# Kernel tuning notes

Measured on AMD Instinct MI355X. Metric: run time of the kernel, lower is better.

## Reference

```python
import jax, jax.numpy as jnp
import numpy as np

B, S, D = 2, 2048, 2048
H, G = 32, 8            # n_head, n_kv_groups
DH = D // H             # 64
HG = H // G             # heads per group = 4


def setup_inputs() -> dict:
    key = jax.random.key(0)
    ks = jax.random.split(key, 7)
    kv_dim = G * DH
    return {
        "q": jax.random.normal(ks[0], (B, S, D), jnp.float32),
        "k": jax.random.normal(ks[1], (B, S, D), jnp.float32),
        "v": jax.random.normal(ks[2], (B, S, D), jnp.float32),
        "mask": jnp.tril(jnp.ones((S, S), jnp.bool_)),  # causal
        "w_q": jax.random.normal(ks[3], (D, D), jnp.float32) * 0.02,
        "w_k": jax.random.normal(ks[4], (kv_dim, D), jnp.float32) * 0.02,
        "w_v": jax.random.normal(ks[5], (kv_dim, D), jnp.float32) * 0.02,
        "w_out": jax.random.normal(ks[6], (D, D), jnp.float32) * 0.02,
    }


def reference(q, k, v, mask, w_q, w_k, w_v, w_out):
    scale = 1.0 / np.sqrt(DH).astype(np.float32)
    # projections (F.linear: x @ W.T)
    qp = (q @ w_q.T).reshape(B, S, G, HG, DH)   # [b s g h d]
    kp = (k @ w_k.T).reshape(B, S, G, DH)       # [b t g d]
    vp = (v @ w_v.T).reshape(B, S, G, DH)
    # grouped attention scores [b g h s t]
    scores = jnp.einsum('bsghd,btgd->bghst', qp, kp) * scale
    scores = jnp.where(mask[None, None, None], scores, jnp.float32(-jnp.inf))
    attn = jax.nn.softmax(scores, axis=-1)
    out = jnp.einsum('bghst,btgd->bsghd', attn, vp).reshape(B, S, D)
    return out @ w_out.T
```

## Files before the change

### kernel.cpp

```cpp
#include <hip/hip_runtime.h>
#include <hip/hip_bf16.h>
#include <stdint.h>

#define B_SZ 2
#define S_LEN 2048
#define D_MODEL 2048
#define NH 32
#define NG 8
#define HGRP 4
#define DHEAD 64
#define KV_DIM 512
#define M_TOK 4096
#define KVB 64
#define QBLK 256

typedef __attribute__((ext_vector_type(8))) short bf16x8;
typedef __attribute__((ext_vector_type(4))) float f32x4;
typedef __attribute__((ext_vector_type(16))) float f32x16;

__device__ inline unsigned short f2bf(float x) {
    uint32_t u = __builtin_bit_cast(uint32_t, x);
    uint32_t r = (u + 0x7fffu + ((u >> 16) & 1u)) >> 16;
    return (unsigned short)r;
}

__device__ inline uint32_t cvtpk(float lo, float hi) {
    uint32_t r;
    asm("v_cvt_pk_bf16_f32 %0, %1, %2" : "=v"(r) : "v"(lo), "v"(hi));
    return r;
}

__device__ inline void plswap(uint32_t& a, uint32_t& b) {
    asm volatile("v_permlane32_swap_b32 %0, %1" : "+v"(a), "+v"(b));
}

__device__ inline float bf2f(unsigned short u) {
    uint32_t x = ((uint32_t)u) << 16;
    return __builtin_bit_cast(float, x);
}

__device__ inline void async_copy16(const void* g, void* l) {
    __builtin_amdgcn_global_load_lds(
        (const __attribute__((address_space(1))) void*)g,
        (__attribute__((address_space(3))) void*)l,
        16, 0, 0);
}

__device__ inline void gbar() {
    asm volatile("" ::: "memory");
    __builtin_amdgcn_s_barrier();
    asm volatile("" ::: "memory");
}
__device__ inline void lgkm0() {
    asm volatile("s_waitcnt lgkmcnt(0)" ::: "memory");
    __builtin_amdgcn_sched_barrier(0);
}

__global__ __launch_bounds__(256) void cvt_all(const float* __restrict__ q,
                                               const float* __restrict__ k,
                                               const float* __restrict__ v,
                                               const float* __restrict__ wq,
                                               const float* __restrict__ wk,
                                               const float* __restrict__ wv,
                                               const float* __restrict__ wo,
                                               unsigned short* __restrict__ qb,
                                               unsigned short* __restrict__ kb,
                                               unsigned short* __restrict__ vb,
                                               unsigned short* __restrict__ wqb,
                                               unsigned short* __restrict__ wkvb,
                                               unsigned short* __restrict__ wob) {
    const int i = blockIdx.x * 256 + threadIdx.x;
    const float* src; unsigned short* dst; int j;
    if (i < 1048576)      { src = q;  dst = qb;  j = i; }
    else if (i < 2097152) { src = k;  dst = kb;  j = i - 1048576; }
    else if (i < 3145728) { src = v;  dst = vb;  j = i - 2097152; }
    else if (i < 3670016) { src = wq; dst = wqb; j = i - 3145728; }
    else if (i < 3801088) { src = wk; dst = wkvb; j = i - 3670016; }
    else if (i < 3932160) { src = wv; dst = wkvb + (size_t)KV_DIM * D_MODEL; j = i - 3801088; }
    else                  { src = wo; dst = wob; j = i - 3932160; }
    const float4* p = reinterpret_cast<const float4*>(src) + (size_t)j * 2;
    float4 a = p[0], b = p[1];
    union { unsigned short u[8]; uint4 v4; } r;
    r.u[0] = f2bf(a.x); r.u[1] = f2bf(a.y); r.u[2] = f2bf(a.z); r.u[3] = f2bf(a.w);
    r.u[4] = f2bf(b.x); r.u[5] = f2bf(b.y); r.u[6] = f2bf(b.z); r.u[7] = f2bf(b.w);
    reinterpret_cast<uint4*>(dst)[j] = r.v4;
}

#define SCALE_Q 0.1803368867f
#define GK 2048

__global__ __launch_bounds__(512, 2) void gemm8p(const unsigned short* __restrict__ Aq,
                                                 const unsigned short* __restrict__ Ak,
                                                 const unsigned short* __restrict__ Av,
                                                 const unsigned short* __restrict__ Bq,
                                                 const unsigned short* __restrict__ Bkv,
                                                 unsigned short* __restrict__ out_q,
                                                 unsigned short* __restrict__ out_k,
                                                 unsigned short* __restrict__ out_v) {
    __shared__ __align__(16) char lds[131072];

    const int tid = threadIdx.x;
    const int lane = tid & 63;
    const int w = tid >> 6;
    const int wm = w >> 2, wn = w & 3;
    const int l15 = lane & 15, l4 = lane >> 4;

    int bid = blockIdx.x;
    bid = (bid & 7) * 24 + (bid >> 3);
    const int mb = bid & 15, nb = bid >> 4;
    const int m0 = mb * 256;

    const unsigned short* Ap;
    const unsigned short* Bp;
    int mode = 0, n0q = 0;
    if (nb < 8) {
        Ap = Aq; Bp = Bq + (size_t)(nb * 256) * GK; mode = 0; n0q = nb * 256;
    } else if (nb < 10) {
        Ap = Ak; Bp = Bkv + (size_t)((nb - 8) * 256) * GK; mode = 1; n0q = (nb - 8) * 256;
    } else {
        Ap = Av; Bp = Bkv + (size_t)((nb - 10) * 256 + 512) * GK; mode = 2; n0q = (nb - 10) * 256;
    }

    const int srow = tid >> 3;
    const int gcol = (((tid & 7) * 16) ^ ((srow & 7) << 4)) >> 1;
    char* const myl = lds + tid * 16;

    auto stageA = [&](int tile, int half) {
        char* dst = myl + (tile & 1) * 32768 + half * 16384;
        const unsigned short* src = Ap + (size_t)(m0 + half * 128 + srow) * GK + tile * 64 + gcol;
        async_copy16(src, dst);
        async_copy16(src + (size_t)64 * GK, dst + 8192);
    };
    auto stageB = [&](int tile, int half) {
        char* dst = myl + 65536 + (tile & 1) * 32768 + half * 16384;
        const unsigned short* src = Bp + (size_t)(half * 128 + srow) * GK + tile * 64 + gcol;
        async_copy16(src, dst);
        async_copy16(src + (size_t)64 * GK, dst + 8192);
    };

    bf16x8 af[4][2], bf[4][2];
    auto loadA = [&](int buf, int mhalf) {
        const char* base = lds + buf * 32768;
#pragma unroll
        for (int mi = 0; mi < 4; ++mi) {
            const int r = wm * 128 + mhalf * 64 + mi * 16 + l15;
#pragma unroll
            for (int ks = 0; ks < 2; ++ks)
                af[mi][ks] = *reinterpret_cast<const bf16x8*>(
                    base + r * 128 + ((ks * 64 + l4 * 16) ^ ((r & 7) << 4)));
        }
    };
    auto loadB = [&](int buf, int nhalf) {
        const char* base = lds + 65536 + buf * 32768;
#pragma unroll
        for (int ni2 = 0; ni2 < 2; ++ni2) {
            const int ni = nhalf * 2 + ni2;
            const int r = wn * 64 + ni * 16 + l15;
#pragma unroll
            for (int ks = 0; ks < 2; ++ks)
                bf[ni][ks] = *reinterpret_cast<const bf16x8*>(
                    base + r * 128 + ((ks * 64 + l4 * 16) ^ ((r & 7) << 4)));
        }
    };

    f32x4 acc[8][4] = {};
    auto mfma16 = [&](int mq, int nq) {
        __builtin_amdgcn_s_setprio(1);
#pragma unroll
        for (int mi = 0; mi < 4; ++mi)
#pragma unroll
            for (int ni2 = 0; ni2 < 2; ++ni2)
#pragma unroll
                for (int ks = 0; ks < 2; ++ks)
                    acc[mq * 4 + mi][nq * 2 + ni2] = __builtin_amdgcn_mfma_f32_16x16x32_bf16(
                        af[mi][ks], bf[nq * 2 + ni2][ks], acc[mq * 4 + mi][nq * 2 + ni2], 0, 0, 0);
        __builtin_amdgcn_s_setprio(0);
    };

    stageA(0, 0); stageA(0, 1); stageB(0, 0); stageB(0, 1); stageB(1, 0); stageB(1, 1);
    asm volatile("s_waitcnt vmcnt(4)" ::: "memory");
    gbar();

    for (int i = 0; i < 16; ++i) {
        const int u = 2 * i;
        const bool nl = (i < 15);
        loadA(0, 0); loadB(0, 0); stageA(u + 1, 0);
        gbar(); lgkm0(); mfma16(0, 0); gbar();
        loadB(0, 1); stageA(u + 1, 1);
        gbar(); lgkm0(); mfma16(0, 1); gbar();
        loadA(0, 1); if (nl) stageB(u + 2, 0);
        gbar(); lgkm0(); mfma16(1, 0); gbar();
        if (nl) stageB(u + 2, 1);
        gbar(); mfma16(1, 1);
        if (nl) asm volatile("s_waitcnt vmcnt(4)" ::: "memory");
        else    asm volatile("s_waitcnt vmcnt(0)" ::: "memory");
        gbar();
        loadA(1, 0); loadB(1, 0); if (nl) stageA(u + 2, 0);
        gbar(); lgkm0(); mfma16(0, 0); gbar();
        loadB(1, 1); if (nl) stageA(u + 2, 1);
        gbar(); lgkm0(); mfma16(0, 1); gbar();
        loadA(1, 1); if (nl) stageB(u + 3, 0);
        gbar(); lgkm0(); mfma16(1, 0); gbar();
        if (nl) stageB(u + 3, 1);
        gbar(); mfma16(1, 1);
        if (nl) asm volatile("s_waitcnt vmcnt(4)" ::: "memory");
        gbar();
    }

    if (mode == 0) {
#pragma unroll
        for (int mi = 0; mi < 8; ++mi) {
            const int row = m0 + wm * 128 + mi * 16 + l4 * 4;
#pragma unroll
            for (int ni = 0; ni < 4; ++ni) {
                const int col = n0q + wn * 64 + ni * 16 + l15;
#pragma unroll
                for (int r = 0; r < 4; ++r)
                    out_q[(size_t)(row + r) * D_MODEL + col] = f2bf(acc[mi][ni][r] * SCALE_Q);
            }
        }
    } else if (mode == 1) {
#pragma unroll
        for (int mi = 0; mi < 8; ++mi) {
            const int row = m0 + wm * 128 + mi * 16 + l4 * 4;
#pragma unroll
            for (int ni = 0; ni < 4; ++ni) {
                const int col = n0q + wn * 64 + ni * 16 + l15;
#pragma unroll
                for (int r = 0; r < 4; ++r)
                    out_k[(size_t)(row + r) * KV_DIM + col] = f2bf(acc[mi][ni][r]);
            }
        }
    } else {
        const int bb = m0 >> 11;
#pragma unroll
        for (int mi = 0; mi < 8; ++mi) {
            const int tok = (m0 & 2047) + wm * 128 + mi * 16 + l4 * 4;
#pragma unroll
            for (int ni = 0; ni < 4; ++ni) {
                const int c = n0q + wn * 64 + ni * 16 + l15;
                const int g = c >> 6, dh = c & 63;
                uint2 pk;
                pk.x = cvtpk(acc[mi][ni][0], acc[mi][ni][1]);
                pk.y = cvtpk(acc[mi][ni][2], acc[mi][ni][3]);
                *reinterpret_cast<uint2*>(out_v + (size_t)((bb * NG + g) * DHEAD + dh) * S_LEN + tok) = pk;
            }
        }
    }
}

__global__ __launch_bounds__(512, 1) void gemm8o(const unsigned short* __restrict__ A,
                                                 const unsigned short* __restrict__ B,
                                                 float* __restrict__ C) {
    __shared__ __align__(16) char lds[98304];

    const int tid = threadIdx.x;
    const int lane = tid & 63;
    const int w = tid >> 6;
    const int wm = w >> 1, wn = w & 1;
    const int l15 = lane & 15, l4 = lane >> 4;

    int bid = blockIdx.x;
    bid = (bid & 7) * 32 + (bid >> 3);
    const int mb = bid & 15, nb = bid >> 4;
    const int m0 = mb * 256, n0 = nb * 128;
    const unsigned short* Bp = B + (size_t)n0 * GK;

    const int srow = tid >> 3;
    const int gcol = (((tid & 7) * 16) ^ ((srow & 7) << 4)) >> 1;

    auto stageA = [&](int tile, int half) {
        char* dst = lds + (tile & 1) * 32768 + half * 16384 + tid * 16;
        const unsigned short* src = A + (size_t)(m0 + half * 128 + srow) * GK + tile * 64 + gcol;
        async_copy16(src, dst);
        async_copy16(src + (size_t)64 * GK, dst + 8192);
    };
    auto stageB = [&](int tile, int half) {
        char* dst = lds + 65536 + (tile & 1) * 16384 + half * 8192 + tid * 16;
        const unsigned short* src = Bp + (size_t)(half * 64 + srow) * GK + tile * 64 + gcol;
        async_copy16(src, dst);
    };

    bf16x8 af[2][2], bf[4][2];
    auto loadA2 = [&](int buf, int mhalf) {
        const char* base = lds + buf * 32768;
#pragma unroll
        for (int mi = 0; mi < 2; ++mi) {
            const int r = wm * 64 + mhalf * 32 + mi * 16 + l15;
#pragma unroll
            for (int ks = 0; ks < 2; ++ks)
                af[mi][ks] = *reinterpret_cast<const bf16x8*>(
                    base + r * 128 + ((ks * 64 + l4 * 16) ^ ((r & 7) << 4)));
        }
    };
    auto loadB2 = [&](int buf, int nhalf) {
        const char* base = lds + 65536 + buf * 16384;
#pragma unroll
        for (int ni2 = 0; ni2 < 2; ++ni2) {
            const int ni = nhalf * 2 + ni2;
            const int r = wn * 64 + ni * 16 + l15;
#pragma unroll
            for (int ks = 0; ks < 2; ++ks)
                bf[ni][ks] = *reinterpret_cast<const bf16x8*>(
                    base + r * 128 + ((ks * 64 + l4 * 16) ^ ((r & 7) << 4)));
        }
    };

    f32x4 acc[4][4] = {};
    auto mfma8 = [&](int mq, int nq) {
        __builtin_amdgcn_s_setprio(1);
#pragma unroll
        for (int mi = 0; mi < 2; ++mi)
#pragma unroll
            for (int ni2 = 0; ni2 < 2; ++ni2)
#pragma unroll
                for (int ks = 0; ks < 2; ++ks)
                    acc[mq * 2 + mi][nq * 2 + ni2] = __builtin_amdgcn_mfma_f32_16x16x32_bf16(
                        af[mi][ks], bf[nq * 2 + ni2][ks], acc[mq * 2 + mi][nq * 2 + ni2], 0, 0, 0);
        __builtin_amdgcn_s_setprio(0);
    };

    stageA(0, 0); stageA(0, 1); stageB(0, 0); stageB(0, 1); stageB(1, 0); stageB(1, 1);
    asm volatile("s_waitcnt vmcnt(2)" ::: "memory");
    gbar();

    for (int i = 0; i < 16; ++i) {
        const int u = 2 * i;
        const bool nl = (i < 15);
        loadA2(0, 0); loadB2(0, 0); stageA(u + 1, 0);
        gbar(); lgkm0(); mfma8(0, 0); gbar();
        loadB2(0, 1); stageA(u + 1, 1);
        gbar(); lgkm0(); mfma8(0, 1); gbar();
        loadA2(0, 1); if (nl) stageB(u + 2, 0);
        gbar(); lgkm0(); mfma8(1, 0); gbar();
        if (nl) stageB(u + 2, 1);
        gbar(); mfma8(1, 1);
        if (nl) asm volatile("s_waitcnt vmcnt(2)" ::: "memory");
        else    asm volatile("s_waitcnt vmcnt(0)" ::: "memory");
        gbar();
        loadA2(1, 0); loadB2(1, 0); if (nl) stageA(u + 2, 0);
        gbar(); lgkm0(); mfma8(0, 0); gbar();
        loadB2(1, 1); if (nl) stageA(u + 2, 1);
        gbar(); lgkm0(); mfma8(0, 1); gbar();
        loadA2(1, 1); if (nl) stageB(u + 3, 0);
        gbar(); lgkm0(); mfma8(1, 0); gbar();
        if (nl) stageB(u + 3, 1);
        gbar(); mfma8(1, 1);
        if (nl) asm volatile("s_waitcnt vmcnt(2)" ::: "memory");
        gbar();
    }

#pragma unroll
    for (int mi = 0; mi < 4; ++mi) {
        const int row = m0 + wm * 64 + mi * 16 + l4 * 4;
#pragma unroll
        for (int ni = 0; ni < 4; ++ni) {
            const int col = n0 + wn * 64 + ni * 16 + l15;
#pragma unroll
            for (int r = 0; r < 4; ++r)
                C[(size_t)(row + r) * D_MODEL + col] = acc[mi][ni][r];
        }
    }
}

__constant__ unsigned char sl_qi[16] = {7,7,7,6,6,6,5,5,4,4,3,3,2,2,1,0};
__constant__ unsigned char sl_j0[16] = {0,11,22,0,10,19,0,11,0,10,0,8,0,6,0,0};
__constant__ unsigned char sl_j1[16] = {11,22,32,10,19,28,11,24,10,20,8,16,6,12,8,4};
__constant__ unsigned char sl_pt[16] = {0,1,2,0,1,2,0,1,0,1,0,1,0,1,0,0};

__global__ __launch_bounds__(512, 4) void attn5_kernel(const unsigned short* __restrict__ qp,
                                                       const unsigned short* __restrict__ kp,
                                                       const unsigned short* __restrict__ vpT,
                                                       unsigned short* __restrict__ attn_out,
                                                       unsigned short* __restrict__ partO,
                                                       float* __restrict__ ml) {
    __shared__ __align__(16) unsigned short Ks[2][KVB * 64];
    __shared__ __align__(16) unsigned short Vs[2][KVB * 64];

    const int tid = threadIdx.x;
    const int lane = tid & 63;
    const int w = tid >> 6;
    const int l31 = lane & 31, hi = lane >> 5;
    const int sr = tid >> 3, sc = tid & 7;
    const int sgcol = (((sc * 16) ^ ((sr & 7) << 4)) >> 1);
    char* const kdst0 = (char*)Ks[0] + tid * 16;
    char* const kdst1 = (char*)Ks[1] + tid * 16;
    char* const vdst0 = (char*)Vs[0] + tid * 16;
    char* const vdst1 = (char*)Vs[1] + tid * 16;

    const int item = blockIdx.x;
    const int slot = item >> 6;
    const int bh = item & 63;
    const int qi = sl_qi[slot];
    const int j0 = sl_j0[slot];
    const int j1 = sl_j1[slot];
    const int part = sl_pt[slot];
    const bool merged = (qi >= 2);
    const int b = bh >> 5, head = bh & 31, g = head >> 2;
    const int s0 = qi * QBLK;
    const int m = s0 + w * 32 + l31;
    const int mmin = s0 + w * 32;
    const int mmaxw = mmin + 31;

    bf16x8 qf[4];
    {
        const unsigned short* qrow = qp + (size_t)(b * S_LEN + m) * D_MODEL + head * DHEAD + hi * 8;
#pragma unroll
        for (int k = 0; k < 4; ++k)
            qf[k] = *reinterpret_cast<const bf16x8*>(qrow + k * 16);
    }

    const unsigned short* kbase = kp + (size_t)(b * S_LEN + sr) * KV_DIM + g * DHEAD + sgcol;
    const unsigned short* vbase = vpT + (size_t)((b * NG + g) * DHEAD + sr) * S_LEN + sgcol;

    float mrun = -1e30f, lrun = 0.f;
    f32x16 o0 = {}, o1 = {};

    async_copy16(kbase + (size_t)j0 * KVB * KV_DIM, kdst0);
    async_copy16(vbase + j0 * KVB, vdst0);
    asm volatile("s_waitcnt vmcnt(0)" ::: "memory");
    gbar();

    for (int j = j0; j < j1; ++j) {
        const int cur = (j - j0) & 1;
        const int t0 = j * KVB;
        if (j + 1 < j1) {
            async_copy16(kbase + (size_t)(j + 1) * KVB * KV_DIM, cur ? kdst0 : kdst1);
            async_copy16(vbase + (j + 1) * KVB, cur ? vdst0 : vdst1);
        }

        const bool tt0 = (t0 <= mmaxw);
        const bool tt1 = (t0 + 32 <= mmaxw);
        if (tt0) {
            const char* Kb = (const char*)Ks[cur];
            const char* Vb = (const char*)Vs[cur];
            const int rswz0 = (l31 & 7) << 4;

            f32x16 s0v = {}, s1v = {};
#pragma unroll
            for (int k = 0; k < 4; ++k) {
                const int coff = k * 32 + hi * 16;
                const bf16x8 kf0 = *reinterpret_cast<const bf16x8*>(
                    Kb + l31 * 128 + (coff ^ rswz0));
                s0v = __builtin_amdgcn_mfma_f32_32x32x16_bf16(kf0, qf[k], s0v, 0, 0, 0);
                if (tt1) {
                    const bf16x8 kf1 = *reinterpret_cast<const bf16x8*>(
                        Kb + (32 + l31) * 128 + (coff ^ rswz0));
                    s1v = __builtin_amdgcn_mfma_f32_32x32x16_bf16(kf1, qf[k], s1v, 0, 0, 0);
                }
            }

            const bool msk = (t0 + KVB - 1) > mmin;
            float rmax = -1e30f;
            if (msk) {
#pragma unroll
                for (int r = 0; r < 16; ++r) {
                    const int tloc = (r & 3) + 8 * (r >> 2) + 4 * hi;
                    float v = s0v[r];
                    if (t0 + tloc > m) v = -1e30f;
                    s0v[r] = v;
                    rmax = fmaxf(rmax, v);
                }
                if (tt1) {
#pragma unroll
                    for (int r = 0; r < 16; ++r) {
                        const int tloc = 32 + (r & 3) + 8 * (r >> 2) + 4 * hi;
                        float v = s1v[r];
                        if (t0 + tloc > m) v = -1e30f;
                        s1v[r] = v;
                        rmax = fmaxf(rmax, v);
                    }
                }
            } else {
#pragma unroll
                for (int r = 0; r < 16; ++r)
                    rmax = fmaxf(rmax, s0v[r]);
                if (tt1) {
#pragma unroll
                    for (int r = 0; r < 16; ++r)
                        rmax = fmaxf(rmax, s1v[r]);
                }
            }
            rmax = fmaxf(rmax, __shfl_xor(rmax, 32, 64));
            if (!__all(rmax <= mrun + 8.0f)) {
                const float mnew = fmaxf(mrun, rmax);
                const float corr = __builtin_amdgcn_exp2f(mrun - mnew);
                lrun *= corr;
#pragma unroll
                for (int r = 0; r < 16; ++r) { o0[r] *= corr; o1[r] *= corr; }
                mrun = mnew;
            }
            float rs = 0.f;
#pragma unroll
            for (int r = 0; r < 16; ++r) {
                const float p = __builtin_amdgcn_exp2f(s0v[r] - mrun);
                s0v[r] = p;
                rs += p;
            }
            if (tt1) {
#pragma unroll
                for (int r = 0; r < 16; ++r) {
                    const float p = __builtin_amdgcn_exp2f(s1v[r] - mrun);
                    s1v[r] = p;
                    rs += p;
                }
            }
            rs += __shfl_xor(rs, 32, 64);
            lrun += rs;

#pragma unroll
            for (int c = 0; c < 4; ++c) {
                if (c >= 2 && !tt1) break;
                const f32x16& sv = (c >> 1) ? s1v : s0v;
                const int h8 = (c & 1) * 8;
                uint32_t a0 = cvtpk(sv[h8 + 0], sv[h8 + 1]);
                uint32_t a1 = cvtpk(sv[h8 + 2], sv[h8 + 3]);
                uint32_t b0 = cvtpk(sv[h8 + 4], sv[h8 + 5]);
                uint32_t b1 = cvtpk(sv[h8 + 6], sv[h8 + 7]);
                plswap(a0, b0); plswap(a1, b1);
                union { uint32_t w4[4]; bf16x8 v; } pf;
                pf.w4[0] = a0; pf.w4[1] = a1; pf.w4[2] = b0; pf.w4[3] = b1;
                const int coff = c * 32 + hi * 16;
                const bf16x8 vf0 = *reinterpret_cast<const bf16x8*>(
                    Vb + l31 * 128 + (coff ^ rswz0));
                o0 = __builtin_amdgcn_mfma_f32_32x32x16_bf16(vf0, pf.v, o0, 0, 0, 0);
                const bf16x8 vf1 = *reinterpret_cast<const bf16x8*>(
                    Vb + (32 + l31) * 128 + (coff ^ rswz0));
                o1 = __builtin_amdgcn_mfma_f32_32x32x16_bf16(vf1, pf.v, o1, 0, 0, 0);
            }
        }
        asm volatile("s_waitcnt vmcnt(0)" ::: "memory");
        gbar();
    }

    if (merged) {
        const int base = 2 * (qi - 2) + (qi == 7 ? 1 : 0);
        const int pb = bh * 14 + base + part;
        const int mrow = w * 32 + l31;
        if (hi == 0) {
            ml[pb * 512 + mrow] = mrun;
            ml[pb * 512 + 256 + mrow] = lrun;
        }
        unsigned short* dst = partO + (size_t)pb * 16384 + mrow * 64 + hi * 4;
#pragma unroll
        for (int qd = 0; qd < 4; ++qd) {
            uint2 pk0, pk1;
            pk0.x = cvtpk(o0[4 * qd + 0], o0[4 * qd + 1]);
            pk0.y = cvtpk(o0[4 * qd + 2], o0[4 * qd + 3]);
            pk1.x = cvtpk(o1[4 * qd + 0], o1[4 * qd + 1]);
            pk1.y = cvtpk(o1[4 * qd + 2], o1[4 * qd + 3]);
            *reinterpret_cast<uint2*>(dst + 8 * qd) = pk0;
            *reinterpret_cast<uint2*>(dst + 32 + 8 * qd) = pk1;
        }
    } else {
        const float inv = 1.0f / lrun;
        unsigned short* dst = attn_out + (size_t)(b * S_LEN + m) * D_MODEL + head * DHEAD + hi * 4;
#pragma unroll
        for (int qd = 0; qd < 4; ++qd) {
            uint2 pk0, pk1;
            pk0.x = cvtpk(o0[4 * qd + 0] * inv, o0[4 * qd + 1] * inv);
            pk0.y = cvtpk(o0[4 * qd + 2] * inv, o0[4 * qd + 3] * inv);
            pk1.x = cvtpk(o1[4 * qd + 0] * inv, o1[4 * qd + 1] * inv);
            pk1.y = cvtpk(o1[4 * qd + 2] * inv, o1[4 * qd + 3] * inv);
            *reinterpret_cast<uint2*>(dst + 8 * qd) = pk0;
            *reinterpret_cast<uint2*>(dst + 32 + 8 * qd) = pk1;
        }
    }
}

__global__ __launch_bounds__(512) void merge3_kernel(const unsigned short* __restrict__ partO,
                                                     const float* __restrict__ ml,
                                                     unsigned short* __restrict__ attn_out) {
    const int blk = blockIdx.x;
    const int bh = blk / 6;
    const int qi = 2 + (blk - bh * 6);
    const int np = (qi >= 6) ? 3 : 2;
    const int base = 2 * (qi - 2) + (qi == 7 ? 1 : 0);
    const int pb = bh * 14 + base;
    const int b = bh >> 5, head = bh & 31;
    const int s0 = qi * QBLK;
    const int tid = threadIdx.x;
    const int row = tid >> 1, dh0 = (tid & 1) * 32;

    float m0 = ml[(pb + 0) * 512 + row], l0 = ml[(pb + 0) * 512 + 256 + row];
    float m1 = ml[(pb + 1) * 512 + row], l1 = ml[(pb + 1) * 512 + 256 + row];
    float m2 = -1e30f, l2 = 0.f;
    if (np == 3) { m2 = ml[(pb + 2) * 512 + row]; l2 = ml[(pb + 2) * 512 + 256 + row]; }
    const float M = fmaxf(fmaxf(m0, m1), m2);
    float w0 = __builtin_amdgcn_exp2f(m0 - M);
    float w1 = __builtin_amdgcn_exp2f(m1 - M);
    float w2 = (np == 3) ? __builtin_amdgcn_exp2f(m2 - M) : 0.f;
    const float inv = 1.0f / (l0 * w0 + l1 * w1 + l2 * w2);
    w0 *= inv; w1 *= inv; w2 *= inv;

    const uint4* p0 = reinterpret_cast<const uint4*>(partO + (size_t)(pb + 0) * 16384 + row * 64 + dh0);
    const uint4* p1 = reinterpret_cast<const uint4*>(partO + (size_t)(pb + 1) * 16384 + row * 64 + dh0);
    const uint4* p2 = reinterpret_cast<const uint4*>(partO + (size_t)(pb + 2) * 16384 + row * 64 + dh0);
    unsigned short* dst = attn_out + (size_t)(b * S_LEN + s0 + row) * D_MODEL + head * DHEAD + dh0;
#pragma unroll
    for (int c = 0; c < 4; ++c) {
        union { unsigned short u[8]; uint4 v; } ua, ub, uc, uo;
        ua.v = p0[c]; ub.v = p1[c];
        if (np == 3) uc.v = p2[c];
#pragma unroll
        for (int e = 0; e < 8; e += 2) {
            float x0 = bf2f(ua.u[e]) * w0 + bf2f(ub.u[e]) * w1;
            float x1 = bf2f(ua.u[e + 1]) * w0 + bf2f(ub.u[e + 1]) * w1;
            if (np == 3) {
                x0 += bf2f(uc.u[e]) * w2;
                x1 += bf2f(uc.u[e + 1]) * w2;
            }
            reinterpret_cast<uint32_t*>(uo.u)[e >> 1] = cvtpk(x0, x1);
        }
        reinterpret_cast<uint4*>(dst)[c] = uo.v;
    }
}

extern "C" void kernel_launch(void* const* d_in, const int* in_sizes, int n_in,
                              void* d_out, int out_size, void* d_ws, size_t ws_size,
                              hipStream_t stream) {
    const float* q     = (const float*)d_in[0];
    const float* k     = (const float*)d_in[1];
    const float* v     = (const float*)d_in[2];
    const float* w_q   = (const float*)d_in[4];
    const float* w_k   = (const float*)d_in[5];
    const float* w_v   = (const float*)d_in[6];
    const float* w_out = (const float*)d_in[7];

    char* ws = (char*)d_ws;
    size_t off = 0;
    auto alloc = [&](size_t n) { char* p = ws + off; off += (n + 255) & ~(size_t)255; return p; };
    unsigned short* qb   = (unsigned short*)alloc((size_t)M_TOK * D_MODEL * 2);
    unsigned short* kb   = (unsigned short*)alloc((size_t)M_TOK * D_MODEL * 2);
    unsigned short* vb   = (unsigned short*)alloc((size_t)M_TOK * D_MODEL * 2);
    unsigned short* wqb  = (unsigned short*)alloc((size_t)D_MODEL * D_MODEL * 2);
    unsigned short* wkvb = (unsigned short*)alloc((size_t)2 * KV_DIM * D_MODEL * 2);
    unsigned short* wob  = (unsigned short*)alloc((size_t)D_MODEL * D_MODEL * 2);
    unsigned short* qpb  = (unsigned short*)alloc((size_t)M_TOK * D_MODEL * 2);
    unsigned short* kpb  = (unsigned short*)alloc((size_t)M_TOK * KV_DIM * 2);
    unsigned short* vtb  = (unsigned short*)alloc((size_t)M_TOK * KV_DIM * 2);
    unsigned short* aob  = (unsigned short*)alloc((size_t)M_TOK * D_MODEL * 2);

    cvt_all<<<dim3(17408), dim3(256), 0, stream>>>(q, k, v, w_q, w_k, w_v, w_out,
                                                   qb, kb, vb, wqb, wkvb, wob);

    gemm8p<<<dim3(192), dim3(512), 0, stream>>>(qb, kb, vb, wqb, wkvb, qpb, kpb, vtb);

    attn5_kernel<<<dim3(1024), dim3(512), 0, stream>>>(qpb, kpb, vtb, aob, kb, (float*)qb);
    merge3_kernel<<<dim3(384), dim3(512), 0, stream>>>(kb, (float*)qb, aob);

    gemm8o<<<dim3(256), dim3(512), 0, stream>>>(aob, wob, (float*)d_out);
}
```

Measured before the change: 190.9 us.

## Fuse fp32 activation conversion into projection GEMM and rebalance attention split

Drops the separate fp32-to-bf16 conversion of the q/k/v activations. The projection GEMM now loads fp32 A tiles into registers, packs them to bf16 and writes them to LDS itself, which removes a full read and write of the activations through HBM. The attention work-split table is rebalanced so q-block 5 is split into three parts and q-block 2 is no longer split, with the merge kernel indexing adjusted to match. Softmax max and sum reductions are rewritten as tree reductions. In exchange, the GEMM A path doubles its global read bytes and adds register pressure and synchronous conversion work inside the pipelined loop.

```diff
diff --git a/kernel.cpp b/kernel.cpp
--- a/kernel.cpp
+++ b/kernel.cpp
@@ -56,28 +56,35 @@
     __builtin_amdgcn_sched_barrier(0);
 }
 
-__global__ __launch_bounds__(256) void cvt_all(const float* __restrict__ q,
-                                               const float* __restrict__ k,
-                                               const float* __restrict__ v,
-                                               const float* __restrict__ wq,
-                                               const float* __restrict__ wk,
-                                               const float* __restrict__ wv,
-                                               const float* __restrict__ wo,
-                                               unsigned short* __restrict__ qb,
-                                               unsigned short* __restrict__ kb,
-                                               unsigned short* __restrict__ vb,
-                                               unsigned short* __restrict__ wqb,
-                                               unsigned short* __restrict__ wkvb,
-                                               unsigned short* __restrict__ wob) {
+__device__ inline float vmax16(const f32x16& v) {
+    float a0 = fmaxf(v[0], v[1]), a1 = fmaxf(v[2], v[3]);
+    float a2 = fmaxf(v[4], v[5]), a3 = fmaxf(v[6], v[7]);
+    float a4 = fmaxf(v[8], v[9]), a5 = fmaxf(v[10], v[11]);
+    float a6 = fmaxf(v[12], v[13]), a7 = fmaxf(v[14], v[15]);
+    float b0 = fmaxf(a0, a1), b1 = fmaxf(a2, a3);
+    float b2 = fmaxf(a4, a5), b3 = fmaxf(a6, a7);
+    return fmaxf(fmaxf(b0, b1), fmaxf(b2, b3));
+}
+__device__ inline float vsum16(const f32x16& v) {
+    float a0 = v[0] + v[1], a1 = v[2] + v[3], a2 = v[4] + v[5], a3 = v[6] + v[7];
+    float a4 = v[8] + v[9], a5 = v[10] + v[11], a6 = v[12] + v[13], a7 = v[14] + v[15];
+    float b0 = a0 + a1, b1 = a2 + a3, b2 = a4 + a5, b3 = a6 + a7;
+    return (b0 + b1) + (b2 + b3);
+}
+
+__global__ __launch_bounds__(256) void cvt_w(const float* __restrict__ wq,
+                                             const float* __restrict__ wk,
+                                             const float* __restrict__ wv,
+                                             const float* __restrict__ wo,
+                                             unsigned short* __restrict__ wqb,
+                                             unsigned short* __restrict__ wkvb,
+                                             unsigned short* __restrict__ wob) {
     const int i = blockIdx.x * 256 + threadIdx.x;
     const float* src; unsigned short* dst; int j;
-    if (i < 1048576)      { src = q;  dst = qb;  j = i; }
-    else if (i < 2097152) { src = k;  dst = kb;  j = i - 1048576; }
-    else if (i < 3145728) { src = v;  dst = vb;  j = i - 2097152; }
-    else if (i < 3670016) { src = wq; dst = wqb; j = i - 3145728; }
-    else if (i < 3801088) { src = wk; dst = wkvb; j = i - 3670016; }
-    else if (i < 3932160) { src = wv; dst = wkvb + (size_t)KV_DIM * D_MODEL; j = i - 3801088; }
-    else                  { src = wo; dst = wob; j = i - 3932160; }
+    if (i < 524288)      { src = wq; dst = wqb; j = i; }
+    else if (i < 655360) { src = wk; dst = wkvb; j = i - 524288; }
+    else if (i < 786432) { src = wv; dst = wkvb + (size_t)KV_DIM * D_MODEL; j = i - 655360; }
+    else                 { src = wo; dst = wob; j = i - 786432; }
     const float4* p = reinterpret_cast<const float4*>(src) + (size_t)j * 2;
     float4 a = p[0], b = p[1];
     union { unsigned short u[8]; uint4 v4; } r;
@@ -89,9 +96,9 @@
 #define SCALE_Q 0.1803368867f
 #define GK 2048
 
-__global__ __launch_bounds__(512, 2) void gemm8p(const unsigned short* __restrict__ Aq,
-                                                 const unsigned short* __restrict__ Ak,
-                                                 const unsigned short* __restrict__ Av,
+__global__ __launch_bounds__(512, 2) void gemm8p(const float* __restrict__ Aqf,
+                                                 const float* __restrict__ Akf,
+                                                 const float* __restrict__ Avf,
                                                  const unsigned short* __restrict__ Bq,
                                                  const unsigned short* __restrict__ Bkv,
                                                  unsigned short* __restrict__ out_q,
@@ -110,26 +117,44 @@
     const int mb = bid & 15, nb = bid >> 4;
     const int m0 = mb * 256;
 
-    const unsigned short* Ap;
+    const float* Af;
     const unsigned short* Bp;
     int mode = 0, n0q = 0;
     if (nb < 8) {
-        Ap = Aq; Bp = Bq + (size_t)(nb * 256) * GK; mode = 0; n0q = nb * 256;
+        Af = Aqf; Bp = Bq + (size_t)(nb * 256) * GK; mode = 0; n0q = nb * 256;
     } else if (nb < 10) {
-        Ap = Ak; Bp = Bkv + (size_t)((nb - 8) * 256) * GK; mode = 1; n0q = (nb - 8) * 256;
+        Af = Akf; Bp = Bkv + (size_t)((nb - 8) * 256) * GK; mode = 1; n0q = (nb - 8) * 256;
     } else {
-        Ap = Av; Bp = Bkv + (size_t)((nb - 10) * 256 + 512) * GK; mode = 2; n0q = (nb - 10) * 256;
+        Af = Avf; Bp = Bkv + (size_t)((nb - 10) * 256 + 512) * GK; mode = 2; n0q = (nb - 10) * 256;
     }
 
     const int srow = tid >> 3;
     const int gcol = (((tid & 7) * 16) ^ ((srow & 7) << 4)) >> 1;
     char* const myl = lds + tid * 16;
 
-    auto stageA = [&](int tile, int half) {
-        char* dst = myl + (tile & 1) * 32768 + half * 16384;
-        const unsigned short* src = Ap + (size_t)(m0 + half * 128 + srow) * GK + tile * 64 + gcol;
-        async_copy16(src, dst);
-        async_copy16(src + (size_t)64 * GK, dst + 8192);
+    float4 av[8];
+    auto issueA = [&](int tile) {
+#pragma unroll
+        for (int h = 0; h < 2; ++h)
+#pragma unroll
+            for (int r2 = 0; r2 < 2; ++r2) {
+                const float* s = Af + (size_t)(m0 + h * 128 + srow + r2 * 64) * GK + tile * 64 + gcol;
+                av[(h * 2 + r2) * 2 + 0] = *reinterpret_cast<const float4*>(s);
+                av[(h * 2 + r2) * 2 + 1] = *reinterpret_cast<const float4*>(s + 4);
+            }
+    };
+    auto writeA = [&](int tile) {
+#pragma unroll
+        for (int h = 0; h < 2; ++h)
+#pragma unroll
+            for (int r2 = 0; r2 < 2; ++r2) {
+                const float4 x = av[(h * 2 + r2) * 2 + 0];
+                const float4 y = av[(h * 2 + r2) * 2 + 1];
+                uint4 o;
+                o.x = cvtpk(x.x, x.y); o.y = cvtpk(x.z, x.w);
+                o.z = cvtpk(y.x, y.y); o.w = cvtpk(y.z, y.w);
+                *reinterpret_cast<uint4*>(myl + (tile & 1) * 32768 + h * 16384 + r2 * 8192) = o;
+            }
     };
     auto stageB = [&](int tile, int half) {
         char* dst = myl + 65536 + (tile & 1) * 32768 + half * 16384;
@@ -177,16 +202,18 @@
         __builtin_amdgcn_s_setprio(0);
     };
 
-    stageA(0, 0); stageA(0, 1); stageB(0, 0); stageB(0, 1); stageB(1, 0); stageB(1, 1);
-    asm volatile("s_waitcnt vmcnt(4)" ::: "memory");
+    issueA(0);
+    stageB(0, 0); stageB(0, 1); stageB(1, 0); stageB(1, 1);
+    writeA(0);
+    asm volatile("s_waitcnt vmcnt(4) lgkmcnt(0)" ::: "memory");
     gbar();
 
     for (int i = 0; i < 16; ++i) {
         const int u = 2 * i;
         const bool nl = (i < 15);
-        loadA(0, 0); loadB(0, 0); stageA(u + 1, 0);
+        loadA(0, 0); loadB(0, 0); issueA(u + 1);
         gbar(); lgkm0(); mfma16(0, 0); gbar();
-        loadB(0, 1); stageA(u + 1, 1);
+        loadB(0, 1);
         gbar(); lgkm0(); mfma16(0, 1); gbar();
         loadA(0, 1); if (nl) stageB(u + 2, 0);
         gbar(); lgkm0(); mfma16(1, 0); gbar();
@@ -194,16 +221,22 @@
         gbar(); mfma16(1, 1);
         if (nl) asm volatile("s_waitcnt vmcnt(4)" ::: "memory");
         else    asm volatile("s_waitcnt vmcnt(0)" ::: "memory");
+        writeA(u + 1);
+        asm volatile("s_waitcnt lgkmcnt(0)" ::: "memory");
         gbar();
-        loadA(1, 0); loadB(1, 0); if (nl) stageA(u + 2, 0);
+        loadA(1, 0); loadB(1, 0); if (nl) issueA(u + 2);
         gbar(); lgkm0(); mfma16(0, 0); gbar();
-        loadB(1, 1); if (nl) stageA(u + 2, 1);
+        loadB(1, 1);
         gbar(); lgkm0(); mfma16(0, 1); gbar();
         loadA(1, 1); if (nl) stageB(u + 3, 0);
         gbar(); lgkm0(); mfma16(1, 0); gbar();
         if (nl) stageB(u + 3, 1);
         gbar(); mfma16(1, 1);
-        if (nl) asm volatile("s_waitcnt vmcnt(4)" ::: "memory");
+        if (nl) {
+            asm volatile("s_waitcnt vmcnt(4)" ::: "memory");
+            writeA(u + 2);
+        }
+        asm volatile("s_waitcnt lgkmcnt(0)" ::: "memory");
         gbar();
     }
 
@@ -363,12 +396,13 @@
     }
 }
 
-__constant__ unsigned char sl_qi[16] = {7,7,7,6,6,6,5,5,4,4,3,3,2,2,1,0};
-__constant__ unsigned char sl_j0[16] = {0,11,22,0,10,19,0,11,0,10,0,8,0,6,0,0};
-__constant__ unsigned char sl_j1[16] = {11,22,32,10,19,28,11,24,10,20,8,16,6,12,8,4};
-__constant__ unsigned char sl_pt[16] = {0,1,2,0,1,2,0,1,0,1,0,1,0,1,0,0};
-
-__global__ __launch_bounds__(512, 4) void attn5_kernel(const unsigned short* __restrict__ qp,
+__constant__ unsigned char sl_qi[16] = {7,7,7,6,6,6,5,5,5,4,4,3,3,2,1,0};
+__constant__ unsigned char sl_j0[16] = {0,11,22,0,10,19,0,8,16,0,10,0,8,0,0,0};
+__constant__ unsigned char sl_j1[16] = {11,22,32,10,19,28,8,16,24,10,20,8,16,12,8,4};
+__constant__ unsigned char sl_pt[16] = {0,1,2,0,1,2,0,1,2,0,1,0,1,0,0,0};
+__constant__ unsigned char pb_base[5] = {0,2,4,7,10};
+
+__global__ __launch_bounds__(512, 4) void attn6_kernel(const unsigned short* __restrict__ qp,
                                                        const unsigned short* __restrict__ kp,
                                                        const unsigned short* __restrict__ vpT,
                                                        unsigned short* __restrict__ attn_out,
@@ -395,7 +429,7 @@
     const int j0 = sl_j0[slot];
     const int j1 = sl_j1[slot];
     const int part = sl_pt[slot];
-    const bool merged = (qi >= 2);
+    const bool merged = (qi >= 3);
     const int b = bh >> 5, head = bh & 31, g = head >> 2;
     const int s0 = qi * QBLK;
     const int m = s0 + w * 32 + l31;
@@ -451,36 +485,22 @@
             }
 
             const bool msk = (t0 + KVB - 1) > mmin;
-            float rmax = -1e30f;
             if (msk) {
 #pragma unroll
                 for (int r = 0; r < 16; ++r) {
                     const int tloc = (r & 3) + 8 * (r >> 2) + 4 * hi;
-                    float v = s0v[r];
-                    if (t0 + tloc > m) v = -1e30f;
-                    s0v[r] = v;
-                    rmax = fmaxf(rmax, v);
+                    if (t0 + tloc > m) s0v[r] = -1e30f;
                 }
                 if (tt1) {
 #pragma unroll
                     for (int r = 0; r < 16; ++r) {
                         const int tloc = 32 + (r & 3) + 8 * (r >> 2) + 4 * hi;
-                        float v = s1v[r];
-                        if (t0 + tloc > m) v = -1e30f;
-                        s1v[r] = v;
-                        rmax = fmaxf(rmax, v);
+                        if (t0 + tloc > m) s1v[r] = -1e30f;
                     }
                 }
-            } else {
-#pragma unroll
-                for (int r = 0; r < 16; ++r)
-                    rmax = fmaxf(rmax, s0v[r]);
-                if (tt1) {
-#pragma unroll
-                    for (int r = 0; r < 16; ++r)
-                        rmax = fmaxf(rmax, s1v[r]);
-                }
-            }
+            }
+            float rmax = vmax16(s0v);
+            if (tt1) rmax = fmaxf(rmax, vmax16(s1v));
             rmax = fmaxf(rmax, __shfl_xor(rmax, 32, 64));
             if (!__all(rmax <= mrun + 8.0f)) {
                 const float mnew = fmaxf(mrun, rmax);
@@ -490,21 +510,16 @@
                 for (int r = 0; r < 16; ++r) { o0[r] *= corr; o1[r] *= corr; }
                 mrun = mnew;
             }
-            float rs = 0.f;
-#pragma unroll
-            for (int r = 0; r < 16; ++r) {
-                const float p = __builtin_amdgcn_exp2f(s0v[r] - mrun);
-                s0v[r] = p;
-                rs += p;
-            }
+#pragma unroll
+            for (int r = 0; r < 16; ++r)
+                s0v[r] = __builtin_amdgcn_exp2f(s0v[r] - mrun);
             if (tt1) {
 #pragma unroll
-                for (int r = 0; r < 16; ++r) {
-                    const float p = __builtin_amdgcn_exp2f(s1v[r] - mrun);
-                    s1v[r] = p;
-                    rs += p;
-                }
-            }
+                for (int r = 0; r < 16; ++r)
+                    s1v[r] = __builtin_amdgcn_exp2f(s1v[r] - mrun);
+            }
+            float rs = vsum16(s0v);
+            if (tt1) rs += vsum16(s1v);
             rs += __shfl_xor(rs, 32, 64);
             lrun += rs;
 
@@ -534,8 +549,7 @@
     }
 
     if (merged) {
-        const int base = 2 * (qi - 2) + (qi == 7 ? 1 : 0);
-        const int pb = bh * 14 + base + part;
+        const int pb = bh * 13 + pb_base[qi - 3] + part;
         const int mrow = w * 32 + l31;
         if (hi == 0) {
             ml[pb * 512 + mrow] = mrun;
@@ -568,15 +582,14 @@
     }
 }
 
-__global__ __launch_bounds__(512) void merge3_kernel(const unsigned short* __restrict__ partO,
+__global__ __launch_bounds__(512) void merge4_kernel(const unsigned short* __restrict__ partO,
                                                      const float* __restrict__ ml,
                                                      unsigned short* __restrict__ attn_out) {
     const int blk = blockIdx.x;
-    const int bh = blk / 6;
-    const int qi = 2 + (blk - bh * 6);
-    const int np = (qi >= 6) ? 3 : 2;
-    const int base = 2 * (qi - 2) + (qi == 7 ? 1 : 0);
-    const int pb = bh * 14 + base;
+    const int bh = blk / 5;
+    const int qi = 3 + (blk - bh * 5);
+    const int np = (qi >= 5) ? 3 : 2;
+    const int pb = bh * 13 + pb_base[qi - 3];
     const int b = bh >> 5, head = bh & 31;
     const int s0 = qi * QBLK;
     const int tid = threadIdx.x;
@@ -630,9 +643,9 @@
     char* ws = (char*)d_ws;
     size_t off = 0;
     auto alloc = [&](size_t n) { char* p = ws + off; off += (n + 255) & ~(size_t)255; return p; };
-    unsigned short* qb   = (unsigned short*)alloc((size_t)M_TOK * D_MODEL * 2);
-    unsigned short* kb   = (unsigned short*)alloc((size_t)M_TOK * D_MODEL * 2);
-    unsigned short* vb   = (unsigned short*)alloc((size_t)M_TOK * D_MODEL * 2);
+    unsigned short* scr1 = (unsigned short*)alloc((size_t)M_TOK * D_MODEL * 2);
+    unsigned short* scr2 = (unsigned short*)alloc((size_t)M_TOK * D_MODEL * 2);
+    unsigned short* scr3 = (unsigned short*)alloc((size_t)M_TOK * D_MODEL * 2);
     unsigned short* wqb  = (unsigned short*)alloc((size_t)D_MODEL * D_MODEL * 2);
     unsigned short* wkvb = (unsigned short*)alloc((size_t)2 * KV_DIM * D_MODEL * 2);
     unsigned short* wob  = (unsigned short*)alloc((size_t)D_MODEL * D_MODEL * 2);
@@ -640,14 +653,14 @@
     unsigned short* kpb  = (unsigned short*)alloc((size_t)M_TOK * KV_DIM * 2);
     unsigned short* vtb  = (unsigned short*)alloc((size_t)M_TOK * KV_DIM * 2);
     unsigned short* aob  = (unsigned short*)alloc((size_t)M_TOK * D_MODEL * 2);
-
-    cvt_all<<<dim3(17408), dim3(256), 0, stream>>>(q, k, v, w_q, w_k, w_v, w_out,
-                                                   qb, kb, vb, wqb, wkvb, wob);
-
-    gemm8p<<<dim3(192), dim3(512), 0, stream>>>(qb, kb, vb, wqb, wkvb, qpb, kpb, vtb);
-
-    attn5_kernel<<<dim3(1024), dim3(512), 0, stream>>>(qpb, kpb, vtb, aob, kb, (float*)qb);
-    merge3_kernel<<<dim3(384), dim3(512), 0, stream>>>(kb, (float*)qb, aob);
+    (void)scr3;
+
+    cvt_w<<<dim3(5120), dim3(256), 0, stream>>>(w_q, w_k, w_v, w_out, wqb, wkvb, wob);
+
+    gemm8p<<<dim3(192), dim3(512), 0, stream>>>(q, k, v, wqb, wkvb, qpb, kpb, vtb);
+
+    attn6_kernel<<<dim3(1024), dim3(512), 0, stream>>>(qpb, kpb, vtb, aob, scr2, (float*)scr1);
+    merge4_kernel<<<dim3(320), dim3(512), 0, stream>>>(scr2, (float*)scr1, aob);
 
     gemm8o<<<dim3(256), dim3(512), 0, stream>>>(aob, wob, (float*)d_out);
 }
```

After: 223.4 us. 1.17x slower.
